# Performance work log

Hardware: AMD Instinct MI355X
Metric: run time of the kernel (lower is better)

The kernel has to match this reference:

```python
import jax, jax.numpy as jnp
import numpy as np

# dims: L = 1 + H*W tokens (cls first), BT = B*T clips*frames
L, BT, D = 577, 128, 768
B, T = 16, 8
H = W = 24
CM = 192   # d_middle = D // REDUCTION(4)
CR = 48    # CM // rf_r(4)
K = 3      # rf_k and spatial kernel


def setup_inputs() -> dict:
    key = jax.random.key(0)
    ks = jax.random.split(key, 10)
    return {
        "x":      jax.random.normal(ks[0], (L, BT, D), jnp.float32),
        # tada_pre_proj: Linear(D -> CM)
        "w_pre":  jax.random.normal(ks[1], (D, CM), jnp.float32) * 0.02,
        "b_pre":  jnp.zeros((CM,), jnp.float32),
        # TAdaConv2dV2 base depthwise weight (1x3x3, groups=CM) and bias
        "w_base": jax.random.normal(ks[2], (K, K, 1, CM), jnp.float32) * 0.1,
        "b_conv": jnp.zeros((CM,), jnp.float32),
        # route function: global 1x1 branch, temporal conv a (CM->CR), temporal conv b (CR->CM, small init)
        "w_g":    jax.random.normal(ks[3], (CM, CM), jnp.float32) * 0.02,
        "b_g":    jnp.zeros((CM,), jnp.float32),
        "w_a":    jax.random.normal(ks[4], (K, CM, CR), jnp.float32) * 0.05,
        "b_a":    jnp.zeros((CR,), jnp.float32),
        "w_b":    jax.random.normal(ks[5], (K, CR, CM), jnp.float32) * 0.02,
        # tada_proj: Linear(CM -> D)
        "w_proj": jax.random.normal(ks[6], (CM, D), jnp.float32) * 0.02,
        "b_proj": jnp.zeros((D,), jnp.float32),
    }


def reference(x, w_pre, b_pre, w_base, b_conv, w_g, b_g, w_a, b_a, w_b, w_proj, b_proj):
    # --- tada_pre_proj ---
    h = x @ w_pre + b_pre                                   # [L, BT, CM]
    cls_tok, sp = h[:1], h[1:]                              # cls token bypasses the conv
    sp = sp.transpose(1, 0, 2).reshape(BT, H, W, CM)        # [BT, H, W, CM]

    # --- route function: per-frame, per-channel calibration alpha ---
    d = sp.reshape(B, T, H * W, CM).mean(axis=2)            # spatial avg pool -> [B, T, CM]
    g = d.mean(axis=1) @ w_g + b_g                          # global temporal descriptor [B, CM]
    a = jax.lax.conv_general_dilated(d + g[:, None, :], w_a, (1,), 'SAME',
                                     dimension_numbers=('NWC', 'WIO', 'NWC')) + b_a
    a = jax.nn.relu(a)                                      # [B, T, CR]
    alpha = jax.lax.conv_general_dilated(a, w_b, (1,), 'SAME',
                                         dimension_numbers=('NWC', 'WIO', 'NWC')) + 1.0  # [B, T, CM]

    # --- calibrated depthwise conv (cal_dim='cout') ---
    # conv2d(x, alpha * W_base) == alpha * conv2d(x, W_base) for depthwise cout calibration
    y = jax.lax.conv_general_dilated(sp, w_base, (1, 1), 'SAME',
                                     dimension_numbers=('NHWC', 'HWIO', 'NHWC'),
                                     feature_group_count=CM)
    y = y * alpha.reshape(BT, 1, 1, CM) + b_conv            # [BT, H, W, CM]
    y = y.reshape(BT, H * W, CM).transpose(1, 0, 2)         # [HW, BT, CM]
    out = jnp.concatenate([cls_tok, y], axis=0)             # [L, BT, CM]

    # --- QuickGELU + tada_proj ---
    out = out * jax.nn.sigmoid(1.702 * out)
    return out @ w_proj + b_proj                            # [L, BT, D]
```

## Files before the change

kernel.cpp:

```cpp
#include <hip/hip_runtime.h>

#define DEV __device__ __forceinline__

typedef short bf16x8 __attribute__((ext_vector_type(8)));
typedef float f32x4  __attribute__((ext_vector_type(4)));
typedef unsigned short ushort_t;


DEV unsigned short f2bf(float f) {
  unsigned u = __float_as_uint(f);
  unsigned r = (u + 0x7fffu + ((u >> 16) & 1u)) >> 16;
  return (unsigned short)r;
}

DEV unsigned cvt_pk_bf16(float a, float b) {
  unsigned r;
  asm("v_cvt_pk_bf16_f32 %0, %1, %2" : "=v"(r) : "v"(a), "v"(b));
  return r;
}

DEV float bf2f(unsigned short b) { return __uint_as_float((unsigned)b << 16); }

DEV float silu_g(float v) { return v / (1.f + __expf(-1.702f * v)); }

DEV void gload_lds16(const void* g, void* l) {
  __builtin_amdgcn_global_load_lds(
      (const __attribute__((address_space(1))) unsigned int*)g,
      (__attribute__((address_space(3))) unsigned int*)l, 16, 0, 0);
}

__global__ __launch_bounds__(256)
void prep_kernel(const float* __restrict__ w_pre, const float* __restrict__ w_proj,
                 short* __restrict__ w_preT, short* __restrict__ w_projT) {
  int i = blockIdx.x * 256 + threadIdx.x;
  if (i < 192 * 768) {
    int n = i / 768, k = i - n * 768;
    w_preT[i] = (short)f2bf(w_pre[k * 192 + n]);
    int n2 = i / 192, k2 = i - n2 * 192;
    w_projT[i] = (short)f2bf(w_proj[k2 * 768 + n2]);
  }
}

template<bool A_BF16, int KTOT, int NTOT, bool OUT_BF16, bool NT_STORE>
__global__ __launch_bounds__(512, 4)
void gemm_kernel(const void* __restrict__ A_, const short* __restrict__ Bt,
                 const float* __restrict__ bias, void* __restrict__ C_) {
  constexpr int BM = 128, BN = 192, BK = 64;
  constexpr int NT = KTOT / BK;
  __shared__ short As[2][BM * BK];
  __shared__ short Bs[2][BN * BK];

  const int tid  = threadIdx.x;
  const int wave = tid >> 6, lane = tid & 63;
  const int m0 = blockIdx.x * BM;
  const int n0 = blockIdx.y * BN;
  const int wm = wave >> 2, wn = wave & 3;
  const int lr  = lane & 15;
  const int lk8 = lane >> 4;
  const int srow = lane >> 3;
  const int schunk = lane & 7;

  const float* Af = (const float*)A_;
  const short* Ab = (const short*)A_;

  f32x4 acc[4][3] = {};
  float4 areg[2][2];

  auto loadA_f32 = [&](int kt) {
    #pragma unroll
    for (int s = 0; s < 2; ++s) {
      int id = tid + s * 512;
      int r = id >> 3, c = id & 7;
      int cg = c ^ (r & 7);
      const float* p = Af + (size_t)(m0 + r) * KTOT + kt + cg * 8;
      areg[s][0] = *(const float4*)p;
      areg[s][1] = *(const float4*)(p + 4);
    }
  };
  auto cvtStoreA = [&](int buf) {
    #pragma unroll
    for (int s = 0; s < 2; ++s) {
      int id = tid + s * 512;
      int r = id >> 3, c = id & 7;
      int4 w;
      w.x = (int)cvt_pk_bf16(areg[s][0].x, areg[s][0].y);
      w.y = (int)cvt_pk_bf16(areg[s][0].z, areg[s][0].w);
      w.z = (int)cvt_pk_bf16(areg[s][1].x, areg[s][1].y);
      w.w = (int)cvt_pk_bf16(areg[s][1].z, areg[s][1].w);
      *(int4*)&As[buf][r * 64 + c * 8] = w;
    }
  };
  auto stageA16 = [&](int kt, int buf) {
    #pragma unroll
    for (int j = 0; j < 2; ++j) {
      int rb8 = wave * 2 + j;
      int r = rb8 * 8 + srow;
      const short* src = Ab + (size_t)(m0 + r) * KTOT + kt + (schunk ^ srow) * 8;
      gload_lds16(src, (char*)As[buf] + rb8 * 1024);
    }
  };
  auto stageB = [&](int kt, int buf) {
    #pragma unroll
    for (int j = 0; j < 3; ++j) {
      int rb8 = wave * 3 + j;
      int r = rb8 * 8 + srow;
      const short* src = Bt + (size_t)(n0 + r) * KTOT + kt + (schunk ^ srow) * 8;
      gload_lds16(src, (char*)Bs[buf] + rb8 * 1024);
    }
  };
  auto compute = [&](int buf) {
    #pragma unroll
    for (int ks = 0; ks < 2; ++ks) {
      int kc = ks * 4 + lk8;
      bf16x8 af[4], bfv[3];
      #pragma unroll
      for (int fm = 0; fm < 4; ++fm) {
        int row = wm * 64 + fm * 16 + lr;
        af[fm] = *(const bf16x8*)&As[buf][row * 64 + (kc ^ (row & 7)) * 8];
      }
      #pragma unroll
      for (int fn = 0; fn < 3; ++fn) {
        int row = wn * 48 + fn * 16 + lr;
        bfv[fn] = *(const bf16x8*)&Bs[buf][row * 64 + (kc ^ (row & 7)) * 8];
      }
      #pragma unroll
      for (int fm = 0; fm < 4; ++fm)
        #pragma unroll
        for (int fn = 0; fn < 3; ++fn)
          acc[fm][fn] = __builtin_amdgcn_mfma_f32_16x16x32_bf16(
              bfv[fn], af[fm], acc[fm][fn], 0, 0, 0);
    }
  };

  if constexpr (!A_BF16) { loadA_f32(0); cvtStoreA(0); }
  else                   stageA16(0, 0);
  stageB(0, 0);
  if constexpr (!A_BF16) { if (NT > 1) loadA_f32(BK); }
  __syncthreads();

  #pragma unroll
  for (int t = 0; t < NT; ++t) {
    const int cur = t & 1, nxt = cur ^ 1;
    if (t + 1 < NT) {
      if constexpr (!A_BF16) {
        cvtStoreA(nxt);
        if (t + 2 < NT) loadA_f32((t + 2) * BK);
      } else {
        stageA16((t + 1) * BK, nxt);
      }
      stageB((t + 1) * BK, nxt);
    }
    compute(cur);
    if (t + 1 < NT) __syncthreads();
  }

  const int cb = (lane >> 4) * 4;
  #pragma unroll
  for (int fm = 0; fm < 4; ++fm) {
    int row = m0 + wm * 64 + fm * 16 + lr;
    #pragma unroll
    for (int fn = 0; fn < 3; ++fn) {
      int col = n0 + wn * 48 + fn * 16 + cb;
      float4 bv = *(const float4*)(bias + col);
      float o0 = acc[fm][fn][0] + bv.x;
      float o1 = acc[fm][fn][1] + bv.y;
      float o2 = acc[fm][fn][2] + bv.z;
      float o3 = acc[fm][fn][3] + bv.w;
      if constexpr (OUT_BF16) {
        ushort_t* Cb = (ushort_t*)C_;
        int2 w;
        w.x = (int)cvt_pk_bf16(o0, o1);
        w.y = (int)cvt_pk_bf16(o2, o3);
        *(int2*)&Cb[(size_t)row * NTOT + col] = w;
      } else {
        float* Cf = (float*)C_;
        f32x4 o; o[0] = o0; o[1] = o1; o[2] = o2; o[3] = o3;
        f32x4* dst = (f32x4*)&Cf[(size_t)row * NTOT + col];
        if constexpr (NT_STORE) __builtin_nontemporal_store(o, dst);
        else                    *dst = o;
      }
    }
  }
}

__global__ __launch_bounds__(192)
void reduce_d_kernel(const ushort_t* __restrict__ h, float* __restrict__ d) {
  const int bt = blockIdx.x, tid = threadIdx.x;
  const int slice = tid / 24, c8 = tid % 24;
  __shared__ float part[8][192];
  float sum[8] = {};
  #pragma unroll 4
  for (int i = 0; i < 72; ++i) {
    int l = 1 + slice * 72 + i;
    bf16x8 v = *(const bf16x8*)&h[((size_t)l * 128 + bt) * 192 + c8 * 8];
    #pragma unroll
    for (int j = 0; j < 8; ++j) sum[j] += bf2f((unsigned short)v[j]);
  }
  #pragma unroll
  for (int j = 0; j < 8; ++j) part[slice][c8 * 8 + j] = sum[j];
  __syncthreads();
  float s = 0.f;
  #pragma unroll
  for (int sl = 0; sl < 8; ++sl) s += part[sl][tid];
  d[bt * 192 + tid] = s * (1.f / 576.f);
}

__global__ __launch_bounds__(256)
void small_path_kernel(const float* __restrict__ d,
                       const float* __restrict__ w_g, const float* __restrict__ b_g,
                       const float* __restrict__ w_a, const float* __restrict__ b_a,
                       const float* __restrict__ w_b,
                       float* __restrict__ alpha) {
  const int b = blockIdx.x, tid = threadIdx.x;
  __shared__ unsigned short wbuf[36864];
  __shared__ float e[8][192];
  __shared__ float md[192];
  __shared__ float a[8][48];

  #pragma unroll
  for (int it = 0; it < 36; ++it) {
    int i = tid + it * 256;
    float4 v = *(const float4*)(w_g + i * 4);
    int2 w;
    w.x = (int)cvt_pk_bf16(v.x, v.y);
    w.y = (int)cvt_pk_bf16(v.z, v.w);
    *(int2*)&wbuf[i * 4] = w;
  }
  for (int i = tid; i < 384; i += 256)
    *(float4*)((float*)e + i * 4) = *(const float4*)(d + (size_t)b * 1536 + i * 4);
  __syncthreads();

  if (tid < 192) {
    float m = 0.f;
    #pragma unroll
    for (int t = 0; t < 8; ++t) m += e[t][tid];
    md[tid] = m * 0.125f;
  }
  __syncthreads();

  if (tid < 192) {
    float accg = b_g[tid];
    #pragma unroll 8
    for (int k = 0; k < 192; ++k)
      accg += md[k] * bf2f(wbuf[k * 192 + tid]);
    #pragma unroll
    for (int t = 0; t < 8; ++t) e[t][tid] += accg;
  }
  __syncthreads();

  #pragma unroll
  for (int it = 0; it < 27; ++it) {
    int i = tid + it * 256;
    float4 v = *(const float4*)(w_a + i * 4);
    int2 w;
    w.x = (int)cvt_pk_bf16(v.x, v.y);
    w.y = (int)cvt_pk_bf16(v.z, v.w);
    *(int2*)&wbuf[i * 4] = w;
  }
  __syncthreads();

  for (int o = tid; o < 384; o += 256) {
    int t = o / 48, r = o - t * 48;
    float acc = b_a[r];
    #pragma unroll
    for (int dt = 0; dt < 3; ++dt) {
      int tt = t + dt - 1;
      if ((unsigned)tt < 8u) {
        #pragma unroll 8
        for (int k = 0; k < 192; ++k)
          acc += e[tt][k] * bf2f(wbuf[(dt * 192 + k) * 48 + r]);
      }
    }
    a[t][r] = fmaxf(acc, 0.f);
  }
  __syncthreads();

  #pragma unroll
  for (int it = 0; it < 27; ++it) {
    int i = tid + it * 256;
    float4 v = *(const float4*)(w_b + i * 4);
    int2 w;
    w.x = (int)cvt_pk_bf16(v.x, v.y);
    w.y = (int)cvt_pk_bf16(v.z, v.w);
    *(int2*)&wbuf[i * 4] = w;
  }
  __syncthreads();

  if (tid < 192) {
    #pragma unroll
    for (int t = 0; t < 8; ++t) {
      float acc = 1.0f;
      #pragma unroll
      for (int dt = 0; dt < 3; ++dt) {
        int tt = t + dt - 1;
        if ((unsigned)tt < 8u) {
          #pragma unroll 8
          for (int r = 0; r < 48; ++r)
            acc += a[tt][r] * bf2f(wbuf[(dt * 48 + r) * 192 + tid]);
        }
      }
      alpha[(size_t)(b * 8 + t) * 192 + tid] = acc;
    }
  }
}

__global__ __launch_bounds__(256)
void dwconv_silu_kernel(const ushort_t* __restrict__ h, const float* __restrict__ alpha,
                        const float* __restrict__ w_base, const float* __restrict__ b_conv,
                        ushort_t* __restrict__ s) {
  const int bt = blockIdx.x, c0 = blockIdx.y * 32;
  const int tid = threadIdx.x;
  __shared__ ushort_t tile[576][32];

  #pragma unroll
  for (int it = 0; it < 9; ++it) {
    int gidx = tid + it * 256;
    int p = gidx >> 2, cc = (gidx & 3) * 8;
    *(bf16x8*)&tile[p][cc] =
        *(const bf16x8*)&h[((size_t)(1 + p) * 128 + bt) * 192 + c0 + cc];
  }

  const int c = tid & 31;
  const int prow = tid >> 5;
  float wv[3][3];
  #pragma unroll
  for (int dh = 0; dh < 3; ++dh)
    #pragma unroll
    for (int dw = 0; dw < 3; ++dw)
      wv[dh][dw] = w_base[(dh * 3 + dw) * 192 + c0 + c];
  const float av = alpha[bt * 192 + c0 + c];
  const float bc = b_conv[c0 + c];

  if (tid < 32) {
    float v = bf2f(h[(size_t)bt * 192 + c0 + tid]);
    s[(size_t)bt * 192 + c0 + tid] = f2bf(silu_g(v));
  }
  __syncthreads();

  for (int i = 0; i < 72; ++i) {
    int p = prow + i * 8;
    int hh = p / 24, ww = p - hh * 24;
    float acc = 0.f;
    #pragma unroll
    for (int dh = 0; dh < 3; ++dh) {
      int y = hh + dh - 1;
      if ((unsigned)y >= 24u) continue;
      #pragma unroll
      for (int dw = 0; dw < 3; ++dw) {
        int xx = ww + dw - 1;
        if ((unsigned)xx >= 24u) continue;
        acc += bf2f(tile[y * 24 + xx][c]) * wv[dh][dw];
      }
    }
    float pre = acc * av + bc;
    s[(size_t)((1 + p) * 128 + bt) * 192 + c0 + c] = f2bf(silu_g(pre));
  }
}

extern "C" void kernel_launch(void* const* d_in, const int* in_sizes, int n_in,
                              void* d_out, int out_size, void* d_ws, size_t ws_size,
                              hipStream_t stream) {
  (void)in_sizes; (void)n_in; (void)out_size; (void)ws_size;
  const float* x      = (const float*)d_in[0];
  const float* w_pre  = (const float*)d_in[1];
  const float* b_pre  = (const float*)d_in[2];
  const float* w_base = (const float*)d_in[3];
  const float* b_conv = (const float*)d_in[4];
  const float* w_g    = (const float*)d_in[5];
  const float* b_g    = (const float*)d_in[6];
  const float* w_a    = (const float*)d_in[7];
  const float* b_a    = (const float*)d_in[8];
  const float* w_b    = (const float*)d_in[9];
  const float* w_proj = (const float*)d_in[10];
  const float* b_proj = (const float*)d_in[11];

  float* out = (float*)d_out;
  ushort_t* h = (ushort_t*)d_out;
  char* ws = (char*)d_ws;
  short* w_preT  = (short*)(ws);
  short* w_projT = (short*)(ws + 294912);
  float* dbuf    = (float*)(ws + 589824);
  float* alpha   = (float*)(ws + 688128);
  short* s       = (short*)(ws + 786432);

  prep_kernel<<<576, 256, 0, stream>>>(w_pre, w_proj, w_preT, w_projT);

  gemm_kernel<false, 768, 192, true, false><<<dim3(577, 1), 512, 0, stream>>>(
      x, w_preT, b_pre, h);

  reduce_d_kernel<<<128, 192, 0, stream>>>(h, dbuf);
  small_path_kernel<<<16, 256, 0, stream>>>(dbuf, w_g, b_g, w_a, b_a, w_b, alpha);
  dwconv_silu_kernel<<<dim3(128, 6), 256, 0, stream>>>(h, alpha, w_base, b_conv,
                                                       (ushort_t*)s);

  gemm_kernel<true, 192, 768, false, true><<<dim3(577, 4), 512, 0, stream>>>(
      s, w_projT, b_proj, out);
}
```

Baseline: 247.1 us.

## Specialize GEMMs with manual waitcnt pipelining and prefetch all K tiles in proj GEMM

Splits the templated GEMM into two specialized kernels. The pre-projection GEMM issues the B stage before the A conversion and uses explicit vmcnt waits plus raw barriers in place of __syncthreads, so loads that are still in flight need not drain. The output GEMM loads all three K tiles up front into triple-buffered LDS and computes each tile as it arrives, which raises LDS use per block and may lower occupancy. It also doubles the threads in the spatial-mean reduction and gives the small route kernel separate weight buffers so weight loads can overlap with compute.

After: 250.7 us. About the same (+1.5%).

```diff
diff --git a/kernel.cpp b/kernel.cpp
--- a/kernel.cpp
+++ b/kernel.cpp
@@ -41,14 +41,129 @@
   }
 }
 
-template<bool A_BF16, int KTOT, int NTOT, bool OUT_BF16, bool NT_STORE>
 __global__ __launch_bounds__(512, 4)
-void gemm_kernel(const void* __restrict__ A_, const short* __restrict__ Bt,
-                 const float* __restrict__ bias, void* __restrict__ C_) {
-  constexpr int BM = 128, BN = 192, BK = 64;
-  constexpr int NT = KTOT / BK;
+void gemm1_kernel(const float* __restrict__ Af, const short* __restrict__ Bt,
+                  const float* __restrict__ bias, ushort_t* __restrict__ C) {
+  constexpr int BM = 128, BN = 192, BK = 64, KTOT = 768, NTOT = 192, NT = 12;
   __shared__ short As[2][BM * BK];
   __shared__ short Bs[2][BN * BK];
+
+  const int tid  = threadIdx.x;
+  const int wave = tid >> 6, lane = tid & 63;
+  const int m0 = blockIdx.x * BM;
+  const int wm = wave >> 2, wn = wave & 3;
+  const int lr  = lane & 15;
+  const int lk8 = lane >> 4;
+  const int srow = lane >> 3;
+  const int schunk = lane & 7;
+
+  f32x4 acc[4][3] = {};
+  float4 areg[2][2];
+
+  auto loadA_f32 = [&](int kt) {
+    #pragma unroll
+    for (int s = 0; s < 2; ++s) {
+      int id = tid + s * 512;
+      int r = id >> 3, c = id & 7;
+      int cg = c ^ (r & 7);
+      const float* p = Af + (size_t)(m0 + r) * KTOT + kt + cg * 8;
+      areg[s][0] = *(const float4*)p;
+      areg[s][1] = *(const float4*)(p + 4);
+    }
+  };
+  auto cvtStoreA = [&](int buf) {
+    #pragma unroll
+    for (int s = 0; s < 2; ++s) {
+      int id = tid + s * 512;
+      int r = id >> 3, c = id & 7;
+      int4 w;
+      w.x = (int)cvt_pk_bf16(areg[s][0].x, areg[s][0].y);
+      w.y = (int)cvt_pk_bf16(areg[s][0].z, areg[s][0].w);
+      w.z = (int)cvt_pk_bf16(areg[s][1].x, areg[s][1].y);
+      w.w = (int)cvt_pk_bf16(areg[s][1].z, areg[s][1].w);
+      *(int4*)&As[buf][r * 64 + c * 8] = w;
+    }
+  };
+  auto stageB = [&](int kt, int buf) {
+    #pragma unroll
+    for (int j = 0; j < 3; ++j) {
+      int rb8 = wave * 3 + j;
+      int r = rb8 * 8 + srow;
+      const short* src = Bt + (size_t)r * KTOT + kt + (schunk ^ srow) * 8;
+      gload_lds16(src, (char*)Bs[buf] + rb8 * 1024);
+    }
+  };
+  auto compute = [&](int buf) {
+    #pragma unroll
+    for (int ks = 0; ks < 2; ++ks) {
+      int kc = ks * 4 + lk8;
+      bf16x8 af[4], bfv[3];
+      #pragma unroll
+      for (int fm = 0; fm < 4; ++fm) {
+        int row = wm * 64 + fm * 16 + lr;
+        af[fm] = *(const bf16x8*)&As[buf][row * 64 + (kc ^ (row & 7)) * 8];
+      }
+      #pragma unroll
+      for (int fn = 0; fn < 3; ++fn) {
+        int row = wn * 48 + fn * 16 + lr;
+        bfv[fn] = *(const bf16x8*)&Bs[buf][row * 64 + (kc ^ (row & 7)) * 8];
+      }
+      #pragma unroll
+      for (int fm = 0; fm < 4; ++fm)
+        #pragma unroll
+        for (int fn = 0; fn < 3; ++fn)
+          acc[fm][fn] = __builtin_amdgcn_mfma_f32_16x16x32_bf16(
+              bfv[fn], af[fm], acc[fm][fn], 0, 0, 0);
+    }
+  };
+
+  loadA_f32(0);
+  cvtStoreA(0);
+  stageB(0, 0);
+  loadA_f32(BK);
+  asm volatile("s_waitcnt vmcnt(4) lgkmcnt(0)" ::: "memory");
+  __builtin_amdgcn_s_barrier();
+
+  #pragma unroll
+  for (int t = 0; t < NT; ++t) {
+    const int cur = t & 1, nxt = cur ^ 1;
+    if (t + 1 < NT) {
+      stageB((t + 1) * BK, nxt);
+      cvtStoreA(nxt);
+      if (t + 2 < NT) loadA_f32((t + 2) * BK);
+    }
+    compute(cur);
+    if (t + 1 < NT) {
+      if (t + 2 < NT)
+        asm volatile("s_waitcnt vmcnt(4) lgkmcnt(0)" ::: "memory");
+      else
+        asm volatile("s_waitcnt vmcnt(0) lgkmcnt(0)" ::: "memory");
+      __builtin_amdgcn_s_barrier();
+    }
+  }
+
+  const int cb = (lane >> 4) * 4;
+  #pragma unroll
+  for (int fm = 0; fm < 4; ++fm) {
+    int row = m0 + wm * 64 + fm * 16 + lr;
+    #pragma unroll
+    for (int fn = 0; fn < 3; ++fn) {
+      int col = wn * 48 + fn * 16 + cb;
+      float4 bv = *(const float4*)(bias + col);
+      int2 w;
+      w.x = (int)cvt_pk_bf16(acc[fm][fn][0] + bv.x, acc[fm][fn][1] + bv.y);
+      w.y = (int)cvt_pk_bf16(acc[fm][fn][2] + bv.z, acc[fm][fn][3] + bv.w);
+      *(int2*)&C[(size_t)row * NTOT + col] = w;
+    }
+  }
+}
+
+__global__ __launch_bounds__(512)
+void gemm2_kernel(const short* __restrict__ Ab, const short* __restrict__ Bt,
+                  const float* __restrict__ bias, float* __restrict__ C) {
+  constexpr int BM = 128, BN = 192, BK = 64, KTOT = 192, NTOT = 768;
+  __shared__ short As[3][BM * BK];
+  __shared__ short Bs[3][BN * BK];
 
   const int tid  = threadIdx.x;
   const int wave = tid >> 6, lane = tid & 63;
@@ -60,54 +175,27 @@
   const int srow = lane >> 3;
   const int schunk = lane & 7;
 
-  const float* Af = (const float*)A_;
-  const short* Ab = (const short*)A_;
-
   f32x4 acc[4][3] = {};
-  float4 areg[2][2];
-
-  auto loadA_f32 = [&](int kt) {
-    #pragma unroll
-    for (int s = 0; s < 2; ++s) {
-      int id = tid + s * 512;
-      int r = id >> 3, c = id & 7;
-      int cg = c ^ (r & 7);
-      const float* p = Af + (size_t)(m0 + r) * KTOT + kt + cg * 8;
-      areg[s][0] = *(const float4*)p;
-      areg[s][1] = *(const float4*)(p + 4);
-    }
-  };
-  auto cvtStoreA = [&](int buf) {
-    #pragma unroll
-    for (int s = 0; s < 2; ++s) {
-      int id = tid + s * 512;
-      int r = id >> 3, c = id & 7;
-      int4 w;
-      w.x = (int)cvt_pk_bf16(areg[s][0].x, areg[s][0].y);
-      w.y = (int)cvt_pk_bf16(areg[s][0].z, areg[s][0].w);
-      w.z = (int)cvt_pk_bf16(areg[s][1].x, areg[s][1].y);
-      w.w = (int)cvt_pk_bf16(areg[s][1].z, areg[s][1].w);
-      *(int4*)&As[buf][r * 64 + c * 8] = w;
-    }
-  };
-  auto stageA16 = [&](int kt, int buf) {
+
+  #pragma unroll
+  for (int tt = 0; tt < 3; ++tt) {
+    int kt = tt * BK;
     #pragma unroll
     for (int j = 0; j < 2; ++j) {
       int rb8 = wave * 2 + j;
       int r = rb8 * 8 + srow;
       const short* src = Ab + (size_t)(m0 + r) * KTOT + kt + (schunk ^ srow) * 8;
-      gload_lds16(src, (char*)As[buf] + rb8 * 1024);
-    }
-  };
-  auto stageB = [&](int kt, int buf) {
+      gload_lds16(src, (char*)As[tt] + rb8 * 1024);
+    }
     #pragma unroll
     for (int j = 0; j < 3; ++j) {
       int rb8 = wave * 3 + j;
       int r = rb8 * 8 + srow;
       const short* src = Bt + (size_t)(n0 + r) * KTOT + kt + (schunk ^ srow) * 8;
-      gload_lds16(src, (char*)Bs[buf] + rb8 * 1024);
-    }
-  };
+      gload_lds16(src, (char*)Bs[tt] + rb8 * 1024);
+    }
+  }
+
   auto compute = [&](int buf) {
     #pragma unroll
     for (int ks = 0; ks < 2; ++ks) {
@@ -132,27 +220,15 @@
     }
   };
 
-  if constexpr (!A_BF16) { loadA_f32(0); cvtStoreA(0); }
-  else                   stageA16(0, 0);
-  stageB(0, 0);
-  if constexpr (!A_BF16) { if (NT > 1) loadA_f32(BK); }
-  __syncthreads();
-
-  #pragma unroll
-  for (int t = 0; t < NT; ++t) {
-    const int cur = t & 1, nxt = cur ^ 1;
-    if (t + 1 < NT) {
-      if constexpr (!A_BF16) {
-        cvtStoreA(nxt);
-        if (t + 2 < NT) loadA_f32((t + 2) * BK);
-      } else {
-        stageA16((t + 1) * BK, nxt);
-      }
-      stageB((t + 1) * BK, nxt);
-    }
-    compute(cur);
-    if (t + 1 < NT) __syncthreads();
-  }
+  asm volatile("s_waitcnt vmcnt(10)" ::: "memory");
+  __builtin_amdgcn_s_barrier();
+  compute(0);
+  asm volatile("s_waitcnt vmcnt(5)" ::: "memory");
+  __builtin_amdgcn_s_barrier();
+  compute(1);
+  asm volatile("s_waitcnt vmcnt(0)" ::: "memory");
+  __builtin_amdgcn_s_barrier();
+  compute(2);
 
   const int cb = (lane >> 4) * 4;
   #pragma unroll
@@ -162,36 +238,25 @@
     for (int fn = 0; fn < 3; ++fn) {
       int col = n0 + wn * 48 + fn * 16 + cb;
       float4 bv = *(const float4*)(bias + col);
-      float o0 = acc[fm][fn][0] + bv.x;
-      float o1 = acc[fm][fn][1] + bv.y;
-      float o2 = acc[fm][fn][2] + bv.z;
-      float o3 = acc[fm][fn][3] + bv.w;
-      if constexpr (OUT_BF16) {
-        ushort_t* Cb = (ushort_t*)C_;
-        int2 w;
-        w.x = (int)cvt_pk_bf16(o0, o1);
-        w.y = (int)cvt_pk_bf16(o2, o3);
-        *(int2*)&Cb[(size_t)row * NTOT + col] = w;
-      } else {
-        float* Cf = (float*)C_;
-        f32x4 o; o[0] = o0; o[1] = o1; o[2] = o2; o[3] = o3;
-        f32x4* dst = (f32x4*)&Cf[(size_t)row * NTOT + col];
-        if constexpr (NT_STORE) __builtin_nontemporal_store(o, dst);
-        else                    *dst = o;
-      }
-    }
-  }
-}
-
-__global__ __launch_bounds__(192)
+      f32x4 o;
+      o[0] = acc[fm][fn][0] + bv.x;
+      o[1] = acc[fm][fn][1] + bv.y;
+      o[2] = acc[fm][fn][2] + bv.z;
+      o[3] = acc[fm][fn][3] + bv.w;
+      __builtin_nontemporal_store(o, (f32x4*)&C[(size_t)row * NTOT + col]);
+    }
+  }
+}
+
+__global__ __launch_bounds__(384)
 void reduce_d_kernel(const ushort_t* __restrict__ h, float* __restrict__ d) {
   const int bt = blockIdx.x, tid = threadIdx.x;
   const int slice = tid / 24, c8 = tid % 24;
-  __shared__ float part[8][192];
+  __shared__ float part[16][192];
   float sum[8] = {};
   #pragma unroll 4
-  for (int i = 0; i < 72; ++i) {
-    int l = 1 + slice * 72 + i;
+  for (int i = 0; i < 36; ++i) {
+    int l = 1 + slice * 36 + i;
     bf16x8 v = *(const bf16x8*)&h[((size_t)l * 128 + bt) * 192 + c8 * 8];
     #pragma unroll
     for (int j = 0; j < 8; ++j) sum[j] += bf2f((unsigned short)v[j]);
@@ -199,10 +264,12 @@
   #pragma unroll
   for (int j = 0; j < 8; ++j) part[slice][c8 * 8 + j] = sum[j];
   __syncthreads();
-  float s = 0.f;
-  #pragma unroll
-  for (int sl = 0; sl < 8; ++sl) s += part[sl][tid];
-  d[bt * 192 + tid] = s * (1.f / 576.f);
+  if (tid < 192) {
+    float s = 0.f;
+    #pragma unroll
+    for (int sl = 0; sl < 16; ++sl) s += part[sl][tid];
+    d[bt * 192 + tid] = s * (1.f / 576.f);
+  }
 }
 
 __global__ __launch_bounds__(256)
@@ -212,7 +279,8 @@
                        const float* __restrict__ w_b,
                        float* __restrict__ alpha) {
   const int b = blockIdx.x, tid = threadIdx.x;
-  __shared__ unsigned short wbuf[36864];
+  __shared__ unsigned short wg_buf[36864];
+  __shared__ unsigned short wa_buf[27648];
   __shared__ float e[8][192];
   __shared__ float md[192];
   __shared__ float a[8][48];
@@ -224,30 +292,8 @@
     int2 w;
     w.x = (int)cvt_pk_bf16(v.x, v.y);
     w.y = (int)cvt_pk_bf16(v.z, v.w);
-    *(int2*)&wbuf[i * 4] = w;
-  }
-  for (int i = tid; i < 384; i += 256)
-    *(float4*)((float*)e + i * 4) = *(const float4*)(d + (size_t)b * 1536 + i * 4);
-  __syncthreads();
-
-  if (tid < 192) {
-    float m = 0.f;
-    #pragma unroll
-    for (int t = 0; t < 8; ++t) m += e[t][tid];
-    md[tid] = m * 0.125f;
-  }
-  __syncthreads();
-
-  if (tid < 192) {
-    float accg = b_g[tid];
-    #pragma unroll 8
-    for (int k = 0; k < 192; ++k)
-      accg += md[k] * bf2f(wbuf[k * 192 + tid]);
-    #pragma unroll
-    for (int t = 0; t < 8; ++t) e[t][tid] += accg;
-  }
-  __syncthreads();
-
+    *(int2*)&wg_buf[i * 4] = w;
+  }
   #pragma unroll
   for (int it = 0; it < 27; ++it) {
     int i = tid + it * 256;
@@ -255,23 +301,27 @@
     int2 w;
     w.x = (int)cvt_pk_bf16(v.x, v.y);
     w.y = (int)cvt_pk_bf16(v.z, v.w);
-    *(int2*)&wbuf[i * 4] = w;
-  }
-  __syncthreads();
-
-  for (int o = tid; o < 384; o += 256) {
-    int t = o / 48, r = o - t * 48;
-    float acc = b_a[r];
-    #pragma unroll
-    for (int dt = 0; dt < 3; ++dt) {
-      int tt = t + dt - 1;
-      if ((unsigned)tt < 8u) {
-        #pragma unroll 8
-        for (int k = 0; k < 192; ++k)
-          acc += e[tt][k] * bf2f(wbuf[(dt * 192 + k) * 48 + r]);
-      }
-    }
-    a[t][r] = fmaxf(acc, 0.f);
+    *(int2*)&wa_buf[i * 4] = w;
+  }
+  for (int i = tid; i < 384; i += 256)
+    *(float4*)((float*)e + i * 4) = *(const float4*)(d + (size_t)b * 1536 + i * 4);
+  __syncthreads();
+
+  if (tid < 192) {
+    float m = 0.f;
+    #pragma unroll
+    for (int t = 0; t < 8; ++t) m += e[t][tid];
+    md[tid] = m * 0.125f;
+  }
+  __syncthreads();
+
+  if (tid < 192) {
+    float accg = b_g[tid];
+    #pragma unroll 8
+    for (int k = 0; k < 192; ++k)
+      accg += md[k] * bf2f(wg_buf[k * 192 + tid]);
+    #pragma unroll
+    for (int t = 0; t < 8; ++t) e[t][tid] += accg;
   }
   __syncthreads();
 
@@ -282,7 +332,21 @@
     int2 w;
     w.x = (int)cvt_pk_bf16(v.x, v.y);
     w.y = (int)cvt_pk_bf16(v.z, v.w);
-    *(int2*)&wbuf[i * 4] = w;
+    *(int2*)&wg_buf[i * 4] = w;
+  }
+  for (int o = tid; o < 384; o += 256) {
+    int t = o / 48, r = o - t * 48;
+    float acc = b_a[r];
+    #pragma unroll
+    for (int dt = 0; dt < 3; ++dt) {
+      int tt = t + dt - 1;
+      if ((unsigned)tt < 8u) {
+        #pragma unroll 8
+        for (int k = 0; k < 192; ++k)
+          acc += e[tt][k] * bf2f(wa_buf[(dt * 192 + k) * 48 + r]);
+      }
+    }
+    a[t][r] = fmaxf(acc, 0.f);
   }
   __syncthreads();
 
@@ -296,7 +360,7 @@
         if ((unsigned)tt < 8u) {
           #pragma unroll 8
           for (int r = 0; r < 48; ++r)
-            acc += a[tt][r] * bf2f(wbuf[(dt * 48 + r) * 192 + tid]);
+            acc += a[tt][r] * bf2f(wg_buf[(dt * 48 + r) * 192 + tid]);
         }
       }
       alpha[(size_t)(b * 8 + t) * 192 + tid] = acc;
@@ -385,14 +449,13 @@
 
   prep_kernel<<<576, 256, 0, stream>>>(w_pre, w_proj, w_preT, w_projT);
 
-  gemm_kernel<false, 768, 192, true, false><<<dim3(577, 1), 512, 0, stream>>>(
-      x, w_preT, b_pre, h);
-
-  reduce_d_kernel<<<128, 192, 0, stream>>>(h, dbuf);
+  gemm1_kernel<<<577, 512, 0, stream>>>(x, w_preT, b_pre, h);
+
+  reduce_d_kernel<<<128, 384, 0, stream>>>(h, dbuf);
   small_path_kernel<<<16, 256, 0, stream>>>(dbuf, w_g, b_g, w_a, b_a, w_b, alpha);
   dwconv_silu_kernel<<<dim3(128, 6), 256, 0, stream>>>(h, alpha, w_base, b_conv,
                                                        (ushort_t*)s);
 
-  gemm_kernel<true, 192, 768, false, true><<<dim3(577, 4), 512, 0, stream>>>(
-      s, w_projT, b_proj, out);
-}
+  gemm2_kernel<<<dim3(577, 4), 512, 0, stream>>>((const short*)s, w_projT,
+                                                 b_proj, out);
+}
```
